# Kernel tuning notes

Hardware: AMD Instinct MI355X
Metric: run time of the kernel (lower is better)

The kernel has to match this reference:

```python
import jax, jax.numpy as jnp
from jax import lax
import numpy as np

D_MODEL = 768
D_STATE = 16
D_CONV = 4
EXPAND = 2
D_INNER = EXPAND * D_MODEL
BATCH = 2
SEQ = 512


def setup_inputs() -> dict:
    key = jax.random.key(0)
    ks = jax.random.split(key, 8)
    s = 0.02
    return {
        "x": jax.random.normal(ks[0], (BATCH, SEQ, D_MODEL), jnp.float32),
        "W_in": jax.random.normal(ks[1], (2 * D_INNER, D_MODEL), jnp.float32) * s,
        "conv_w": jax.random.normal(ks[2], (D_INNER, 1, D_CONV), jnp.float32) * s,
        "conv_b": jnp.zeros((D_INNER,), jnp.float32),
        "W_x": jax.random.normal(ks[3], (D_INNER + 2 * D_STATE, D_INNER), jnp.float32) * s,
        "W_dt": jax.random.normal(ks[4], (D_INNER, D_INNER), jnp.float32) * s,
        "b_dt": jnp.zeros((D_INNER,), jnp.float32),
        "A_log": jnp.log(jax.random.uniform(ks[5], (D_INNER, D_STATE), jnp.float32, 1e-4, 1.0)),
        "Dp": jnp.ones((D_INNER,), jnp.float32),
        "W_out": jax.random.normal(ks[6], (D_MODEL, D_INNER), jnp.float32) * s,
    }


def parallel_scan_log(log_coeffs, log_values):
    """Faithful port of ParallelScan.parallel_scan_log (Blelchh-style up/down sweep
    in log space). Indices are static, so the Python loop over O(log L) levels is
    trace-time only."""
    B, L, D = log_coeffs.shape
    if L <= 4:
        run = log_values[:, 0]
        outs = [run]
        for i in range(1, L):
            run = jnp.logaddexp(run, log_coeffs[:, i] + log_values[:, i])
            outs.append(run)
        return jnp.stack(outs, axis=1)
    levels = int(np.ceil(np.log2(L)))
    coeffs, values = log_coeffs, log_values
    # up-sweep
    for level in range(levels):
        step = 2 ** (level + 1)
        if step - 1 >= L:
            break
        right = np.arange(step - 1, L, step)
        left = right - 2 ** level
        m = (left >= 0) & (right < L)
        left, right = left[m], right[m]
        if left.size == 0:
            continue
        new_c = coeffs[:, left] + coeffs[:, right]
        new_v = jnp.logaddexp(values[:, left], coeffs[:, right] + values[:, right])
        coeffs = coeffs.at[:, right].set(new_c)
        values = values.at[:, right].set(new_v)
    # down-sweep
    for level in range(levels - 1, -1, -1):
        step = 2 ** (level + 1)
        if step - 1 >= L:
            continue
        right = np.arange(step - 1, L, step)
        left = right - 2 ** level
        m = (left >= 0) & (right < L)
        left, right = left[m], right[m]
        if left.size == 0:
            continue
        tmp = values[:, right]
        new_r = jnp.logaddexp(values[:, left], coeffs[:, right] + values[:, right])
        values = values.at[:, right].set(new_r)
        values = values.at[:, left].set(tmp)
    return values


def reference(x, W_in, conv_w, conv_b, W_x, W_dt, b_dt, A_log, Dp, W_out):
    Bsz, L, _ = x.shape
    xz = x @ W_in.T                                 # [B, L, 2*d_inner]
    x_inner, z = jnp.split(xz, 2, axis=-1)
    # depthwise causal conv1d (pad left d_conv-1, truncate to L == torch slice)
    xc = jnp.transpose(x_inner, (0, 2, 1))          # [B, d_inner, L]
    xc = lax.conv_general_dilated(
        xc, conv_w, (1,), [(D_CONV - 1, 0)],
        dimension_numbers=("NCH", "OIH", "NCH"),
        feature_group_count=D_INNER)
    xc = xc + conv_b[None, :, None]
    x_conv = jax.nn.silu(jnp.transpose(xc, (0, 2, 1)))  # [B, L, d_inner]
    x_dbl = x_conv @ W_x.T                              # [B, L, d_inner + 2*d_state]
    delta, Bmat, Cmat = jnp.split(x_dbl, [D_INNER, D_INNER + D_STATE], axis=-1)
    delta = jax.nn.softplus(delta @ W_dt.T + b_dt)      # [B, L, d_inner]
    # selective scan
    A = -jnp.exp(A_log)                                 # [d_inner, d_state]
    deltaA = jnp.exp(jnp.einsum("bld,dn->bldn", delta, A))
    deltaB_u = jnp.einsum("bld,bln,bld->bldn", delta, Bmat, x_conv)
    log_coeffs = jnp.log(deltaA + 1e-12).reshape(Bsz, L, -1)
    log_values = jnp.log(jnp.abs(deltaB_u) + 1e-12).reshape(Bsz, L, -1)
    scanned = jnp.exp(parallel_scan_log(log_coeffs, log_values))
    scanned = scanned.reshape(Bsz, L, D_INNER, D_STATE)
    y = jnp.einsum("bldn,bln->bld", scanned, Cmat) + x_conv * Dp
    y = y * jax.nn.silu(z)
    return y @ W_out.T
```

## Files before the change

kernel.cpp:

```cpp
#include <hip/hip_runtime.h>
#include <math.h>

#define D_MODEL 768
#define D_STATE 16
#define D_CONV  4
#define D_INNER 1536
#define BATCH   2
#define SEQ     512
#define M_ROWS  (BATCH * SEQ)
#define N_XZ    (2 * D_INNER)
#define N_XDBL  (D_INNER + 2 * D_STATE)

typedef _Float16 half8 __attribute__((ext_vector_type(8)));
typedef float  f32x4  __attribute__((ext_vector_type(4)));
typedef unsigned short ushort_t;
typedef ushort_t ushort8_t __attribute__((ext_vector_type(8)));

__device__ __forceinline__ ushort_t f2h(float f) {
    _Float16 h = (_Float16)f;
    return *(ushort_t*)&h;
}
__device__ __forceinline__ void pack8(const float* s, ushort_t* d) {
    ushort8_t o;
#pragma unroll
    for (int j = 0; j < 8; ++j) o[j] = f2h(s[j]);
    *(ushort8_t*)d = o;
}
__device__ __forceinline__ void gld16(const ushort_t* g, void* l) {
    __builtin_amdgcn_global_load_lds((const __attribute__((address_space(1))) void*)g,
                                     (__attribute__((address_space(3))) void*)l, 16, 0, 0);
}

#define SX  (M_ROWS * D_MODEL)
#define SW1 (N_XZ * D_MODEL)
#define SW2 (N_XDBL * D_INNER)
__global__ __launch_bounds__(256) void split3_kernel(
    const float* __restrict__ x, const float* __restrict__ win,
    const float* __restrict__ wx,
    ushort_t* __restrict__ xs, ushort_t* __restrict__ w1, ushort_t* __restrict__ w2)
{
    long i = ((long)blockIdx.x * 256 + threadIdx.x) * 8;
    const float* src; ushort_t* dst; long base;
    if (i < SX)            { src = x;   dst = xs; base = i; }
    else if (i < SX + SW1) { src = win; dst = w1; base = i - SX; }
    else                   { src = wx;  dst = w2; base = i - SX - SW1; }
    float v[8];
    *(float4*)(v)     = *(const float4*)(src + base);
    *(float4*)(v + 4) = *(const float4*)(src + base + 4);
    pack8(v, dst + base);
}

#define SWDT (D_INNER * D_INNER)
#define SWO  (D_MODEL * D_INNER)
__global__ __launch_bounds__(256) void split2_kernel(
    const float* __restrict__ wdt, const float* __restrict__ wo,
    ushort_t* __restrict__ w1, ushort_t* __restrict__ wout)
{
    long i = ((long)blockIdx.x * 256 + threadIdx.x) * 8;
    const float* src; ushort_t* dst; long base;
    if (i < SWDT) { src = wdt; dst = w1;   base = i; }
    else          { src = wo;  dst = wout; base = i - SWDT; }
    float v[8];
    *(float4*)(v)     = *(const float4*)(src + base);
    *(float4*)(v + 4) = *(const float4*)(src + base + 4);
    pack8(v, dst + base);
}

__global__ __launch_bounds__(256) void gemm_lds(
    const ushort_t* __restrict__ A, int lda,
    const ushort_t* __restrict__ B, int ldb,
    float* __restrict__ Cbase, long pstride, int ldc,
    int N, int kc)
{
    __shared__ ushort_t smA[2][4096];
    __shared__ ushort_t smB[2][4096];

    const int tid  = threadIdx.x;
    const int w    = tid >> 6;
    const int lane = tid & 63;
    const int lr   = lane & 15;
    const int lq   = lane >> 4;

    const int Gx = gridDim.x, Gy = gridDim.y;
    const int T = Gx * Gy * gridDim.z;
    const int f = blockIdx.x + Gx * (blockIdx.y + Gy * blockIdx.z);
    const int g = (T & 7) ? f : ((f & 7) * (T >> 3) + (f >> 3));
    const int bx = g % Gx;
    const int by = (g / Gx) % Gy;
    const int z  = g / (Gx * Gy);
    float* __restrict__ C = Cbase + (long)z * pstride;

    const int bm = by * 128;
    const int bn = bx * 128;
    const int k0base = z * kc;

    auto stage = [&](int buf, int k0) {
#pragma unroll
        for (int i = 0; i < 2; ++i) {
            const int gA = i * 4 + w;
            const int rA = bm + gA * 16 + lr;
            gld16(A + (long)rA * lda + k0 + lq * 8, &smA[buf][gA * 512]);
        }
#pragma unroll
        for (int i = 0; i < 2; ++i) {
            const int gB = i * 4 + w;
            int rB = bn + gB * 16 + lr; if (rB >= N) rB = N - 1;
            gld16(B + (long)rB * ldb + k0 + lq * 8, &smB[buf][gB * 512]);
        }
    };

    f32x4 acc[4][4] = {};
    const int wm = (w & 1) * 64;
    const int wn = (w >> 1) * 64;

    stage(0, k0base);
    __syncthreads();
    const int nIter = kc >> 5;
    for (int it = 0; it < nIter; ++it) {
        const int buf = it & 1;
        if (it + 1 < nIter) stage(buf ^ 1, k0base + (it + 1) * 32);

        half8 ah[4], bh[4];
#pragma unroll
        for (int mt = 0; mt < 4; ++mt)
            ah[mt] = *(const half8*)&smA[buf][(((w & 1) * 4 + mt) * 512) + lq * 128 + lr * 8];
#pragma unroll
        for (int nt = 0; nt < 4; ++nt)
            bh[nt] = *(const half8*)&smB[buf][(((w >> 1) * 4 + nt) * 512) + lq * 128 + lr * 8];
#pragma unroll
        for (int mt = 0; mt < 4; ++mt)
#pragma unroll
            for (int nt = 0; nt < 4; ++nt)
                acc[mt][nt] = __builtin_amdgcn_mfma_f32_16x16x32_f16(ah[mt], bh[nt], acc[mt][nt], 0, 0, 0);
        __syncthreads();
    }

#pragma unroll
    for (int mt = 0; mt < 4; ++mt)
#pragma unroll
        for (int nt = 0; nt < 4; ++nt)
#pragma unroll
            for (int r = 0; r < 4; ++r) {
                int row = bm + wm + mt * 16 + lq * 4 + r;
                int col = bn + wn + nt * 16 + lr;
                if (col >= N) continue;
                C[(long)row * ldc + col] = acc[mt][nt][r];
            }
}

__global__ __launch_bounds__(256) void conv_silu_kernel(
    const float* __restrict__ p0, const float* __restrict__ p1,
    const float* __restrict__ conv_w,
    const float* __restrict__ conv_b,
    float* __restrict__ xconvT,
    float* __restrict__ zsiluT,
    ushort_t* __restrict__ xc)
{
    int idx = blockIdx.x * blockDim.x + threadIdx.x;
    if (idx >= M_ROWS * D_INNER) return;
    int d = idx % D_INNER;
    int r = idx / D_INNER;
    int l = r % SEQ;
    float acc = conv_b[d];
#pragma unroll
    for (int k = 0; k < D_CONV; ++k) {
        if (l - (D_CONV - 1) + k >= 0) {
            long o = (long)(r - (D_CONV - 1 - k)) * N_XZ + d;
            acc = fmaf(conv_w[d * D_CONV + k], p0[o] + p1[o], acc);
        }
    }
    float s = acc / (1.f + expf(-acc));
    xconvT[(long)d * M_ROWS + r] = s;
    xc[(long)r * D_INNER + d] = f2h(s);
    long oz = (long)r * N_XZ + D_INNER + d;
    float zv = p0[oz] + p1[oz];
    zsiluT[(long)d * M_ROWS + r] = zv / (1.f + expf(-zv));
}

__global__ __launch_bounds__(256) void ep_xdbl_kernel(
    const float* __restrict__ P, long ps,
    ushort_t* __restrict__ xd, float* __restrict__ BCT)
{
    long i = ((long)blockIdx.x * 256 + threadIdx.x) * 8;
    if (i >= (long)M_ROWS * N_XDBL) return;
    int row = (int)(i / N_XDBL);
    int col = (int)(i - (long)row * N_XDBL);
    float f[8];
#pragma unroll
    for (int j = 0; j < 8; ++j) f[j] = P[i + j] + P[i + j + ps] + P[i + j + 2 * ps];
    pack8(f, xd + i);
    if (col >= D_INNER) {
#pragma unroll
        for (int j = 0; j < 8; ++j)
            BCT[(long)(col + j - D_INNER) * M_ROWS + row] = f[j];
    }
}

__global__ __launch_bounds__(256) void ep_merge_kernel(
    const float* __restrict__ P, long ps, float* __restrict__ out)
{
    long i = ((long)blockIdx.x * 256 + threadIdx.x) * 8;
    if (i >= (long)M_ROWS * D_MODEL) return;
    float o[8];
#pragma unroll
    for (int j = 0; j < 8; ++j) {
        float v = 0.f;
#pragma unroll
        for (int z = 0; z < 6; ++z) v += P[i + j + z * ps];
        o[j] = v;
    }
    *(float4*)(out + i)     = *(float4*)(o);
    *(float4*)(out + i + 4) = *(float4*)(o + 4);
}

__global__ __launch_bounds__(256) void scan_kernel(
    const float* __restrict__ P, long ps,
    const float* __restrict__ b_dt,
    const float* __restrict__ xconvT,
    const float* __restrict__ zsiluT,
    const float* __restrict__ BCT,
    const float* __restrict__ A_log,
    const float* __restrict__ Dp,
    float* __restrict__ uT)
{
    const int bid = blockIdx.x;
    const int b   = bid / (D_INNER / 4);
    const int dg  = bid % (D_INNER / 4);
    const int tid = threadIdx.x;
    const int w   = tid >> 6;
    const int t   = tid & 63;
    const int d   = dg * 4 + w;
    const int base = b * SEQ;
    const int l0 = 8 * t;

    const long od = (long)d * M_ROWS + base + l0;
    const float bdt = b_dt[d];
    float dl[8], xr[8], yac[8];
#pragma unroll
    for (int i = 0; i < 8; ++i) {
        float v = P[od + i] + P[od + i + ps] + P[od + i + 2 * ps] + P[od + i + 3 * ps] + bdt;
        dl[i] = fmaxf(v, 0.f) + log1pf(expf(-fabsf(v)));
        xr[i] = xconvT[od + i];
        yac[i] = 0.f;
    }

    for (int n = 0; n < D_STATE; ++n) {
        const float Adn = -expf(A_log[d * D_STATE + n]);
        const float4* Bp = (const float4*)(BCT + (long)n * M_ROWS + base + l0);
        float4 b0 = Bp[0], b1 = Bp[1];
        float Bv[8] = {b0.x, b0.y, b0.z, b0.w, b1.x, b1.y, b1.z, b1.w};
        float c[8], v[8];
#pragma unroll
        for (int i = 0; i < 8; ++i) {
            c[i] = expf(dl[i] * Adn) + 1e-12f;
            v[i] = fabsf(dl[i] * Bv[i] * xr[i]) + 1e-12f;
        }
#pragma unroll
        for (int p = 0; p < 8; p += 2) { v[p+1] = fmaf(c[p+1], v[p+1], v[p]); c[p+1] *= c[p]; }
        v[3] = fmaf(c[3], v[3], v[1]); c[3] *= c[1];
        v[7] = fmaf(c[7], v[7], v[5]); c[7] *= c[5];
        v[7] = fmaf(c[7], v[7], v[3]); c[7] *= c[3];
        float c7 = c[7], v7 = v[7];
#pragma unroll
        for (int h = 1; h <= 32; h <<= 1) {
            float vl = __shfl_up(v7, (unsigned)h);
            float cl = __shfl_up(c7, (unsigned)h);
            bool right = ((t & (2 * h - 1)) == (2 * h - 1));
            if (right) { v7 = fmaf(c7, v7, vl); c7 *= cl; }
        }
#pragma unroll
        for (int h = 32; h >= 1; h >>= 1) {
            float vl = __shfl_up(v7, (unsigned)h);
            float vr = __shfl_down(v7, (unsigned)h);
            bool right = ((t & (2 * h - 1)) == (2 * h - 1));
            bool left  = ((t & (2 * h - 1)) == (h - 1));
            float nv = v7;
            if (right) nv = fmaf(c7, v7, vl);
            if (left)  nv = vr;
            v7 = nv;
        }
        v[7] = v7;
        c[7] = c7;
        float tmp;
        tmp = v[7]; v[7] = fmaf(c[7], v[7], v[3]); v[3] = tmp;
        tmp = v[3]; v[3] = fmaf(c[3], v[3], v[1]); v[1] = tmp;
        tmp = v[7]; v[7] = fmaf(c[7], v[7], v[5]); v[5] = tmp;
#pragma unroll
        for (int p = 0; p < 8; p += 2) {
            tmp = v[p+1]; v[p+1] = fmaf(c[p+1], v[p+1], v[p]); v[p] = tmp;
        }
        const float4* Cp = (const float4*)(BCT + (long)(16 + n) * M_ROWS + base + l0);
        float4 c0 = Cp[0], c1 = Cp[1];
        float Cv[8] = {c0.x, c0.y, c0.z, c0.w, c1.x, c1.y, c1.z, c1.w};
#pragma unroll
        for (int i = 0; i < 8; ++i) yac[i] = fmaf(v[i], Cv[i], yac[i]);
    }

    const float Dpd = Dp[d];
#pragma unroll
    for (int i = 0; i < 8; ++i) {
        float uv = fmaf(xr[i], Dpd, yac[i]) * zsiluT[od + i];
        uT[od + i] = uv;
    }
}

__global__ __launch_bounds__(256) void transpose_split_kernel(
    const float* __restrict__ uT, ushort_t* __restrict__ u)
{
    __shared__ float T[64][65];
    const int m0 = blockIdx.x * 64;
    const int d0 = blockIdx.y * 64;
    const int c  = threadIdx.x & 63;
    const int rr = threadIdx.x >> 6;
#pragma unroll
    for (int p = 0; p < 64; p += 4)
        T[p + rr][c] = uT[(long)(d0 + p + rr) * M_ROWS + m0 + c];
    __syncthreads();
#pragma unroll
    for (int p = 0; p < 64; p += 4) {
        int rm = p + rr;
        float v = T[c][rm];
        u[(long)(m0 + rm) * D_INNER + (d0 + c)] = f2h(v);
    }
}

extern "C" void kernel_launch(void* const* d_in, const int* in_sizes, int n_in,
                              void* d_out, int out_size, void* d_ws, size_t ws_size,
                              hipStream_t stream)
{
    (void)in_sizes; (void)n_in; (void)out_size; (void)ws_size;

    const float* x      = (const float*)d_in[0];
    const float* W_in   = (const float*)d_in[1];
    const float* conv_w = (const float*)d_in[2];
    const float* conv_b = (const float*)d_in[3];
    const float* W_x    = (const float*)d_in[4];
    const float* W_dt   = (const float*)d_in[5];
    const float* b_dt   = (const float*)d_in[6];
    const float* A_log  = (const float*)d_in[7];
    const float* Dp     = (const float*)d_in[8];
    const float* W_out  = (const float*)d_in[9];
    float* out = (float*)d_out;

    float* ws = (float*)d_ws;
    long off = 0;
    float* P      = ws + off; off += 2L * M_ROWS * N_XZ;
    float* xconvT = ws + off; off += (long)D_INNER * M_ROWS;
    float* zsiluT = ws + off; off += (long)D_INNER * M_ROWS;
    float* uT     = ws + off; off += (long)D_INNER * M_ROWS;
    float* xcu    = ws + off; off += (long)M_ROWS * D_INNER / 2;
    float* xsbuf  = ws + off; off += (long)M_ROWS * D_MODEL / 2;
    float* w1buf  = ws + off; off += (long)N_XZ * D_MODEL / 2;
    float* w2buf  = ws + off; off += (long)N_XDBL * D_INNER / 2;
    float* xdbuf  = ws + off; off += (long)M_ROWS * N_XDBL / 2;
    float* BCT    = ws + off; off += (long)2 * D_STATE * M_ROWS;

    ushort_t* xs   = (ushort_t*)xsbuf;
    ushort_t* w1   = (ushort_t*)w1buf;
    ushort_t* w2   = (ushort_t*)w2buf;
    ushort_t* xc   = (ushort_t*)xcu;
    ushort_t* xd   = (ushort_t*)xdbuf;
    ushort_t* u_i  = (ushort_t*)xcu;
    float* P6      = P;

    const long psG4 = (long)D_INNER * M_ROWS;

    dim3 blk(256);

    hipLaunchKernelGGL(split3_kernel, dim3((SX + SW1 + SW2) / 2048), blk, 0, stream,
                       x, W_in, W_x, xs, w1, w2);
    hipLaunchKernelGGL(gemm_lds, dim3(N_XZ / 128, M_ROWS / 128, 2), blk, 0, stream,
                       xs, D_MODEL, w1, D_MODEL,
                       P, (long)M_ROWS * N_XZ, N_XZ, N_XZ, D_MODEL / 2);
    hipLaunchKernelGGL(conv_silu_kernel, dim3((M_ROWS * D_INNER) / 256), blk, 0, stream,
                       P, P + (long)M_ROWS * N_XZ, conv_w, conv_b, xconvT, zsiluT, xc);
    hipLaunchKernelGGL(gemm_lds, dim3((N_XDBL + 127) / 128, M_ROWS / 128, 3), blk, 0, stream,
                       xc, D_INNER, w2, D_INNER,
                       P, (long)M_ROWS * N_XDBL, N_XDBL, N_XDBL, D_INNER / 3);
    hipLaunchKernelGGL(ep_xdbl_kernel, dim3((M_ROWS * N_XDBL) / 2048), blk, 0, stream,
                       P, (long)M_ROWS * N_XDBL, xd, BCT);
    hipLaunchKernelGGL(split2_kernel, dim3((SWDT + SWO) / 2048), blk, 0, stream,
                       W_dt, W_out, w1, w2);
    hipLaunchKernelGGL(gemm_lds, dim3(M_ROWS / 128, D_INNER / 128, 4), blk, 0, stream,
                       w1, D_INNER, xd, N_XDBL,
                       P, psG4, M_ROWS, M_ROWS, D_INNER / 4);
    hipLaunchKernelGGL(scan_kernel, dim3(BATCH * (D_INNER / 4)), blk, 0, stream,
                       P, psG4, b_dt, xconvT, zsiluT, BCT, A_log, Dp, uT);
    hipLaunchKernelGGL(transpose_split_kernel, dim3(M_ROWS / 64, D_INNER / 64), blk, 0, stream,
                       uT, u_i);
    hipLaunchKernelGGL(gemm_lds, dim3(D_MODEL / 128, M_ROWS / 128, 6), blk, 0, stream,
                       u_i, D_INNER, w2, D_INNER,
                       P6, (long)M_ROWS * D_MODEL, D_MODEL, D_MODEL, D_INNER / 6);
    hipLaunchKernelGGL(ep_merge_kernel, dim3((M_ROWS * D_MODEL) / 2048), blk, 0, stream,
                       P6, (long)M_ROWS * D_MODEL, out);
}
```

Before: 237.7 us.

## Split scan state dimension across waves with one block per channel

The selective-scan kernel now launches one block per (batch, channel). Each of the four waves handles four of the sixteen state indices instead of one wave looping over all sixteen, and partial outputs are reduced through shared memory. Loads of delta and x are made coalesced by staging them through an LDS transpose. The Blelloch up/down-sweep is replaced with a Hillis-Steele inclusive scan plus a serial in-thread pass. The kernel also uses __expf and drops the 1e-12 epsilons. This raises parallelism and cuts serial work per thread, at the cost of an extra barrier, a shared-memory reduction and a small numeric deviation.

Result: faster. 223.1 us (-6.1%).

```diff
diff --git a/kernel.cpp b/kernel.cpp
--- a/kernel.cpp
+++ b/kernel.cpp
@@ -223,84 +223,91 @@
     const float* __restrict__ Dp,
     float* __restrict__ uT)
 {
+    __shared__ float dlT[512];
+    __shared__ float xrT[512];
+    __shared__ float red[3 * 512];
+
     const int bid = blockIdx.x;
-    const int b   = bid / (D_INNER / 4);
-    const int dg  = bid % (D_INNER / 4);
+    const int b   = bid / D_INNER;
+    const int d   = bid % D_INNER;
     const int tid = threadIdx.x;
     const int w   = tid >> 6;
     const int t   = tid & 63;
-    const int d   = dg * 4 + w;
-    const int base = b * SEQ;
+    const long od = (long)d * M_ROWS + b * SEQ;
+
+    const float bdt = b_dt[d];
+#pragma unroll
+    for (int q = 0; q < 2; ++q) {
+        const int l = tid + q * 256;
+        float v = P[od + l] + P[od + l + ps] + P[od + l + 2 * ps] + P[od + l + 3 * ps] + bdt;
+        float sp = fmaxf(v, 0.f) + log1pf(expf(-fabsf(v)));
+        const int li = (l & 7) * 64 + (l >> 3);
+        dlT[li] = sp;
+        xrT[li] = xconvT[od + l];
+    }
+    __syncthreads();
+
+    float dl[8], xr[8], dx[8], yac[8];
+#pragma unroll
+    for (int j = 0; j < 8; ++j) {
+        dl[j] = dlT[j * 64 + t];
+        xr[j] = xrT[j * 64 + t];
+        dx[j] = dl[j] * xr[j];
+        yac[j] = 0.f;
+    }
     const int l0 = 8 * t;
 
-    const long od = (long)d * M_ROWS + base + l0;
-    const float bdt = b_dt[d];
-    float dl[8], xr[8], yac[8];
-#pragma unroll
-    for (int i = 0; i < 8; ++i) {
-        float v = P[od + i] + P[od + i + ps] + P[od + i + 2 * ps] + P[od + i + 3 * ps] + bdt;
-        dl[i] = fmaxf(v, 0.f) + log1pf(expf(-fabsf(v)));
-        xr[i] = xconvT[od + i];
-        yac[i] = 0.f;
-    }
-
-    for (int n = 0; n < D_STATE; ++n) {
+#pragma unroll
+    for (int nn = 0; nn < 4; ++nn) {
+        const int n = w * 4 + nn;
         const float Adn = -expf(A_log[d * D_STATE + n]);
-        const float4* Bp = (const float4*)(BCT + (long)n * M_ROWS + base + l0);
+        const float4* Bp = (const float4*)(BCT + (long)n * M_ROWS + b * SEQ + l0);
         float4 b0 = Bp[0], b1 = Bp[1];
         float Bv[8] = {b0.x, b0.y, b0.z, b0.w, b1.x, b1.y, b1.z, b1.w};
         float c[8], v[8];
 #pragma unroll
-        for (int i = 0; i < 8; ++i) {
-            c[i] = expf(dl[i] * Adn) + 1e-12f;
-            v[i] = fabsf(dl[i] * Bv[i] * xr[i]) + 1e-12f;
-        }
-#pragma unroll
-        for (int p = 0; p < 8; p += 2) { v[p+1] = fmaf(c[p+1], v[p+1], v[p]); c[p+1] *= c[p]; }
-        v[3] = fmaf(c[3], v[3], v[1]); c[3] *= c[1];
-        v[7] = fmaf(c[7], v[7], v[5]); c[7] *= c[5];
-        v[7] = fmaf(c[7], v[7], v[3]); c[7] *= c[3];
-        float c7 = c[7], v7 = v[7];
+        for (int j = 0; j < 8; ++j) {
+            c[j] = __expf(dl[j] * Adn);
+            v[j] = fabsf(dx[j] * Bv[j]);
+        }
+        float c01 = c[1] * c[0], v01 = fmaf(c[1], v[0], v[1]);
+        float c23 = c[3] * c[2], v23 = fmaf(c[3], v[2], v[3]);
+        float c45 = c[5] * c[4], v45 = fmaf(c[5], v[4], v[5]);
+        float c67 = c[7] * c[6], v67 = fmaf(c[7], v[6], v[7]);
+        float c03 = c23 * c01,  v03 = fmaf(c23, v01, v23);
+        float c47 = c67 * c45,  v47 = fmaf(c67, v45, v67);
+        float cA  = c47 * c03,  vA  = fmaf(c47, v03, v47);
 #pragma unroll
         for (int h = 1; h <= 32; h <<= 1) {
-            float vl = __shfl_up(v7, (unsigned)h);
-            float cl = __shfl_up(c7, (unsigned)h);
-            bool right = ((t & (2 * h - 1)) == (2 * h - 1));
-            if (right) { v7 = fmaf(c7, v7, vl); c7 *= cl; }
-        }
-#pragma unroll
-        for (int h = 32; h >= 1; h >>= 1) {
-            float vl = __shfl_up(v7, (unsigned)h);
-            float vr = __shfl_down(v7, (unsigned)h);
-            bool right = ((t & (2 * h - 1)) == (2 * h - 1));
-            bool left  = ((t & (2 * h - 1)) == (h - 1));
-            float nv = v7;
-            if (right) nv = fmaf(c7, v7, vl);
-            if (left)  nv = vr;
-            v7 = nv;
-        }
-        v[7] = v7;
-        c[7] = c7;
-        float tmp;
-        tmp = v[7]; v[7] = fmaf(c[7], v[7], v[3]); v[3] = tmp;
-        tmp = v[3]; v[3] = fmaf(c[3], v[3], v[1]); v[1] = tmp;
-        tmp = v[7]; v[7] = fmaf(c[7], v[7], v[5]); v[5] = tmp;
-#pragma unroll
-        for (int p = 0; p < 8; p += 2) {
-            tmp = v[p+1]; v[p+1] = fmaf(c[p+1], v[p+1], v[p]); v[p] = tmp;
-        }
-        const float4* Cp = (const float4*)(BCT + (long)(16 + n) * M_ROWS + base + l0);
+            float cl = __shfl_up(cA, (unsigned)h);
+            float vl = __shfl_up(vA, (unsigned)h);
+            if (t >= h) { vA = fmaf(cA, vl, vA); cA = cA * cl; }
+        }
+        float s = __shfl_up(vA, 1u);
+        if (t == 0) s = 0.f;
+        const float4* Cp = (const float4*)(BCT + (long)(16 + n) * M_ROWS + b * SEQ + l0);
         float4 c0 = Cp[0], c1 = Cp[1];
         float Cv[8] = {c0.x, c0.y, c0.z, c0.w, c1.x, c1.y, c1.z, c1.w};
 #pragma unroll
-        for (int i = 0; i < 8; ++i) yac[i] = fmaf(v[i], Cv[i], yac[i]);
-    }
-
-    const float Dpd = Dp[d];
-#pragma unroll
-    for (int i = 0; i < 8; ++i) {
-        float uv = fmaf(xr[i], Dpd, yac[i]) * zsiluT[od + i];
-        uT[od + i] = uv;
+        for (int j = 0; j < 8; ++j) {
+            s = fmaf(c[j], s, v[j]);
+            yac[j] = fmaf(s, Cv[j], yac[j]);
+        }
+    }
+
+    if (w) {
+#pragma unroll
+        for (int j = 0; j < 8; ++j) red[(w - 1) * 512 + j * 64 + t] = yac[j];
+    }
+    __syncthreads();
+    if (w == 0) {
+        const float Dpd = Dp[d];
+#pragma unroll
+        for (int j = 0; j < 8; ++j) {
+            float y = yac[j] + red[j * 64 + t] + red[512 + j * 64 + t] + red[1024 + j * 64 + t];
+            float uv = fmaf(xr[j], Dpd, y) * zsiluT[od + l0 + j];
+            uT[od + l0 + j] = uv;
+        }
     }
 }
 
@@ -384,7 +391,7 @@
     hipLaunchKernelGGL(gemm_lds, dim3(M_ROWS / 128, D_INNER / 128, 4), blk, 0, stream,
                        w1, D_INNER, xd, N_XDBL,
                        P, psG4, M_ROWS, M_ROWS, D_INNER / 4);
-    hipLaunchKernelGGL(scan_kernel, dim3(BATCH * (D_INNER / 4)), blk, 0, stream,
+    hipLaunchKernelGGL(scan_kernel, dim3(BATCH * D_INNER), blk, 0, stream,
                        P, psG4, b_dt, xconvT, zsiluT, BCT, A_log, Dp, uT);
     hipLaunchKernelGGL(transpose_split_kernel, dim3(M_ROWS / 64, D_INNER / 64), blk, 0, stream,
                        uT, u_i);
```
